# Optimization experiments

Measured on AMD Instinct MI355X. Metric: run time of the kernel, lower is better.

The kernel has to match this reference:

```python
import jax, jax.numpy as jnp
import numpy as np

BLANK = 1
NEG = -1e30


def ctc_loss_mean(logprobs, targets, input_lengths, target_lengths):
    """CTC loss, log-space forward DP, matching torch.nn.CTCLoss(blank=1, reduction='mean').
    logprobs: [B,T,V] log-softmaxed; targets: [B,L] int; lengths: [B] int."""
    B, T, V = logprobs.shape
    L = targets.shape[1]
    S = 2 * L + 1  # extended label seq: blank interleaved
    ext = jnp.full((B, S), BLANK, dtype=targets.dtype)
    ext = ext.at[:, 1::2].set(targets)
    # lp_ext[b,t,s] = logprobs[b,t,ext[b,s]]
    lp_ext = jnp.take_along_axis(logprobs, jnp.broadcast_to(ext[:, None, :], (B, T, S)), axis=2)
    ext_m2 = jnp.pad(ext, ((0, 0), (2, 0)), constant_values=BLANK)[:, :S]
    skip_ok = (ext != BLANK) & (ext != ext_m2)  # [B,S] allow s-2 transition

    alpha = jnp.full((B, S), NEG, dtype=logprobs.dtype)
    alpha = alpha.at[:, 0].set(lp_ext[:, 0, 0])
    alpha = alpha.at[:, 1].set(jnp.where(target_lengths > 0, lp_ext[:, 0, 1], NEG))

    def step(alpha, inp):
        lp_t, t = inp  # lp_t: [B,S]
        a1 = jnp.pad(alpha, ((0, 0), (1, 0)), constant_values=NEG)[:, :S]
        a2 = jnp.pad(alpha, ((0, 0), (2, 0)), constant_values=NEG)[:, :S]
        a2 = jnp.where(skip_ok, a2, NEG)
        new = jnp.logaddexp(jnp.logaddexp(alpha, a1), a2) + lp_t
        alpha = jnp.where((t < input_lengths)[:, None], new, alpha)
        return alpha, None

    lp_tbs = jnp.transpose(lp_ext, (1, 0, 2))  # [T,B,S]
    alpha, _ = jax.lax.scan(step, alpha, (lp_tbs[1:], jnp.arange(1, T)))

    idx_last = 2 * target_lengths  # final blank position
    idx_prev = jnp.maximum(idx_last - 1, 0)
    a_last = jnp.take_along_axis(alpha, idx_last[:, None], axis=1)[:, 0]
    a_prev = jnp.where(target_lengths > 0,
                       jnp.take_along_axis(alpha, idx_prev[:, None], axis=1)[:, 0], NEG)
    per_sample = -jnp.logaddexp(a_last, a_prev)
    tl = jnp.maximum(target_lengths, 1).astype(logprobs.dtype)
    return jnp.mean(per_sample / tl)  # torch 'mean': divide by target_len, then batch mean


def setup_inputs() -> dict:
    key = jax.random.key(0)
    ks = jax.random.split(key, 8)
    B, Ssrc, D, STRIDE, V, L = 32, 512, 512, 4, 512, 256
    representation = jax.random.normal(ks[0], (B, Ssrc, D), dtype=jnp.float32)
    encoder_mask = jnp.ones((B, Ssrc), dtype=bool)
    targets = jax.random.randint(ks[1], (B, L), 2, V)  # avoid blank=1 and 0
    target_mask = jnp.ones((B, L), dtype=bool)
    def lin(k, fin, fout):
        return jax.random.normal(k, (fin, fout), dtype=jnp.float32) / np.sqrt(fin)
    return {
        "representation": representation,
        "encoder_mask": encoder_mask,
        "targets": targets,
        "target_mask": target_mask,
        "W_exp": lin(ks[2], D, STRIDE * D),
        "b_exp": jnp.zeros((STRIDE * D,), jnp.float32),
        "W1": lin(ks[3], D, 2 * D),
        "b1": jnp.zeros((2 * D,), jnp.float32),
        "W2": lin(ks[4], 2 * D, V),
        "b2": jnp.zeros((V,), jnp.float32),
    }


def reference(representation, encoder_mask, targets, target_mask,
              W_exp, b_exp, W1, b1, W2, b2):
    B = representation.shape[0]
    dim = W_exp.shape[0]
    seq_lengths = encoder_mask.astype(jnp.int32).sum(1)
    stride = W_exp.shape[1] // dim
    # expand: Linear(dim, stride*dim) then fold stride into time axis
    states = (jnp.einsum("bsd,de->bse", representation, W_exp) + b_exp).reshape(B, -1, dim)
    h = jax.nn.relu(jnp.einsum("btd,dh->bth", states, W1) + b1)
    logits = jnp.einsum("bth,hv->btv", h, W2) + b2  # dropout: eval-mode identity
    logprobs = jax.nn.log_softmax(logits, axis=-1)
    target_lengths = target_mask.astype(jnp.int32).sum(1)
    out_lengths = stride * seq_lengths
    loss = ctc_loss_mean(logprobs, targets, out_lengths, target_lengths)
    loss = jnp.where(jnp.isnan(loss) | jnp.isinf(loss), jnp.zeros_like(loss), loss)
    return logprobs, out_lengths, loss
```

## Files before the change

### kernel.cpp

```cpp
#include <hip/hip_runtime.h>
#include <math.h>

#define B_ 32
#define SSRC 512
#define D_ 512
#define STRIDE_ 4
#define V_ 512
#define L_ 256
#define T_ (SSRC * STRIDE_)
#define S_ (2 * L_ + 1)
#define BLANKI 1
#define PSTRIDE 264
#define BOOST 4096.0f
#define BOOST_BITS 12

typedef __attribute__((ext_vector_type(8))) short bf16x8;
typedef __attribute__((ext_vector_type(4))) float f32x4;

__device__ __forceinline__ unsigned short bf16r(float x) {
    unsigned u = __float_as_uint(x);
    return (unsigned short)((u + 0x7fffu + ((u >> 16) & 1u)) >> 16);
}
__device__ __forceinline__ float bf2f(unsigned short u) {
    return __uint_as_float((unsigned)u << 16);
}
__device__ __forceinline__ void gl_lds16(const unsigned short* g, unsigned short* l) {
    __builtin_amdgcn_global_load_lds(
        (const __attribute__((address_space(1))) unsigned int*)g,
        (__attribute__((address_space(3))) unsigned int*)l, 16, 0, 0);
}

__global__ __launch_bounds__(256) void combine_bias(
    const float* __restrict__ b_exp, const float* __restrict__ W1,
    const float* __restrict__ b1, float* __restrict__ bc)
{
    int j = blockIdx.x * 256 + threadIdx.x;
    int k = j >> 10, h = j & 1023;
    float s = b1[h];
    const float* be = b_exp + k * 512;
    for (int d = 0; d < 512; ++d)
        s = fmaf(be[d], W1[d * 1024 + h], s);
    bc[j] = s;
}

__global__ __launch_bounds__(256) void transpose_cvt(
    const float* __restrict__ in, unsigned short* __restrict__ out, int R, int C)
{
    __shared__ float tile[32][33];
    int bx = blockIdx.x * 32, by = blockIdx.y * 32;
    int tx = threadIdx.x, ty = threadIdx.y;
#pragma unroll
    for (int i = 0; i < 32; i += 8)
        tile[ty + i][tx] = in[(size_t)(by + ty + i) * C + bx + tx];
    __syncthreads();
#pragma unroll
    for (int i = 0; i < 32; i += 8)
        out[(size_t)(bx + ty + i) * R + by + tx] = bf16r(tile[tx][ty + i]);
}

__global__ __launch_bounds__(256) void cvt_f32_bf16(
    const float* __restrict__ in, unsigned short* __restrict__ out, int n4)
{
    int i = blockIdx.x * 256 + threadIdx.x;
    if (i >= n4) return;
    float4 v = ((const float4*)in)[i];
    ushort4 o;
    o.x = bf16r(v.x); o.y = bf16r(v.y); o.z = bf16r(v.z); o.w = bf16r(v.w);
    ((ushort4*)out)[i] = o;
}

template <bool RELU, bool OUTBF16, bool BIAS>
__global__ __launch_bounds__(256) void gemm_mfma(
    const unsigned short* __restrict__ A, int lda, long zA,
    const unsigned short* __restrict__ BT, int ldb, long zBT,
    void* __restrict__ Cvoid, int ldc, long zC,
    const float* __restrict__ bias, int K)
{
    __shared__ unsigned short As[2][128][32];
    __shared__ unsigned short Bs[2][128][32];
    const int tid = threadIdx.x;
    const int wid = tid >> 6, lane = tid & 63;

    A  += (size_t)blockIdx.z * zA;
    BT += (size_t)blockIdx.z * zBT;
    unsigned short* Cb = OUTBF16 ? ((unsigned short*)Cvoid + (size_t)blockIdx.z * zC) : nullptr;
    float*          Cf = OUTBF16 ? nullptr : ((float*)Cvoid + (size_t)blockIdx.z * zC);

    const int gx = gridDim.x;
    int wg = blockIdx.y * gx + blockIdx.x;
    const int q = (gx * gridDim.y) >> 3;
    wg = (wg & 7) * q + (wg >> 3);
    const int bm = (wg / gx) * 128, bn = (wg % gx) * 128;

    const int wm = (wid >> 1) * 64, wn = (wid & 1) * 64;

    f32x4 acc[4][4] = {};
    const int r_in = lane >> 2;
    const int cch = (lane & 3) * 8;
    const int rbase = wid * 32;

    auto stage = [&](int buf, int k0) {
#pragma unroll
        for (int i = 0; i < 2; ++i) {
            int rloc = rbase + i * 16;
            gl_lds16(A  + (size_t)(bm + rloc + r_in) * lda + k0 + cch, &As[buf][rloc][0]);
            gl_lds16(BT + (size_t)(bn + rloc + r_in) * ldb + k0 + cch, &Bs[buf][rloc][0]);
        }
    };

    const int nt = K / 32;
    stage(0, 0);
    for (int t = 0; t < nt; ++t) {
        int cur = t & 1;
        __syncthreads();
        if (t + 1 < nt) stage(cur ^ 1, (t + 1) * 32);
        bf16x8 af[4], bfr[4];
#pragma unroll
        for (int mi = 0; mi < 4; ++mi)
            af[mi] = *(const bf16x8*)&As[cur][wm + mi * 16 + (lane & 15)][(lane >> 4) * 8];
#pragma unroll
        for (int ni = 0; ni < 4; ++ni)
            bfr[ni] = *(const bf16x8*)&Bs[cur][wn + ni * 16 + (lane & 15)][(lane >> 4) * 8];
#pragma unroll
        for (int mi = 0; mi < 4; ++mi)
#pragma unroll
            for (int ni = 0; ni < 4; ++ni)
                acc[mi][ni] = __builtin_amdgcn_mfma_f32_16x16x32_bf16(
                    af[mi], bfr[ni], acc[mi][ni], 0, 0, 0);
    }

#pragma unroll
    for (int ni = 0; ni < 4; ++ni) {
        int gcol = bn + wn + ni * 16 + (lane & 15);
        float bv = BIAS ? bias[gcol] : 0.f;
#pragma unroll
        for (int mi = 0; mi < 4; ++mi) {
#pragma unroll
            for (int q2 = 0; q2 < 4; ++q2) {
                int grow = bm + wm + mi * 16 + ((lane >> 4) << 2) + q2;
                float x = acc[mi][ni][q2] + bv;
                if (RELU) x = fmaxf(x, 0.f);
                if (OUTBF16)
                    Cb[(size_t)grow * ldc + gcol] = bf16r(x);
                else
                    Cf[(size_t)grow * ldc + gcol] = x;
            }
        }
    }
}

__global__ __launch_bounds__(512) void gemm2_lsm(
    const unsigned short* __restrict__ H,
    const unsigned short* __restrict__ W2T,
    const float* __restrict__ b2,
    float* __restrict__ lp)
{
    __shared__ __align__(16) char SMEM[81920];
    unsigned short* As = (unsigned short*)SMEM;
    unsigned short* Bs = (unsigned short*)(SMEM + 16384);
    float* redm = (float*)SMEM;
    float* reds = (float*)(SMEM + 2048);

    const int tid = threadIdx.x;
    const int wid = tid >> 6, lane = tid & 63;
    const int wr = wid >> 2, wc = wid & 3;
    const int r0 = blockIdx.x * 128;

    auto stage = [&](int buf, int k0) {
#pragma unroll
        for (int ii = 0; ii < 5; ++ii) {
            int issue = wid * 5 + ii;
            if (issue < 8) {
                int rr = issue * 16;
                gl_lds16(H + (size_t)(r0 + rr + (lane >> 2)) * 1024 + k0 + (lane & 3) * 8,
                         &As[buf * 4096 + rr * 32]);
            } else {
                int rr = (issue - 8) * 16;
                gl_lds16(W2T + (size_t)(rr + (lane >> 2)) * 1024 + k0 + (lane & 3) * 8,
                         &Bs[buf * 16384 + rr * 32]);
            }
        }
    };

    f32x4 acc[4][8] = {};
    stage(0, 0);
    for (int t = 0; t < 32; ++t) {
        const int cur = t & 1;
        __syncthreads();
        if (t + 1 < 32) stage(cur ^ 1, (t + 1) * 32);
        bf16x8 af[4], bfr[8];
#pragma unroll
        for (int mi = 0; mi < 4; ++mi)
            af[mi] = *(const bf16x8*)&As[cur * 4096 +
                        (wr * 64 + mi * 16 + (lane & 15)) * 32 + (lane >> 4) * 8];
#pragma unroll
        for (int ni = 0; ni < 8; ++ni)
            bfr[ni] = *(const bf16x8*)&Bs[cur * 16384 +
                        (wc * 128 + ni * 16 + (lane & 15)) * 32 + (lane >> 4) * 8];
#pragma unroll
        for (int mi = 0; mi < 4; ++mi)
#pragma unroll
            for (int ni = 0; ni < 8; ++ni)
                acc[mi][ni] = __builtin_amdgcn_mfma_f32_16x16x32_bf16(
                    af[mi], bfr[ni], acc[mi][ni], 0, 0, 0);
    }

    float bcol[8];
#pragma unroll
    for (int ni = 0; ni < 8; ++ni) bcol[ni] = b2[wc * 128 + ni * 16 + (lane & 15)];
#pragma unroll
    for (int mi = 0; mi < 4; ++mi)
#pragma unroll
        for (int ni = 0; ni < 8; ++ni)
#pragma unroll
            for (int q = 0; q < 4; ++q) acc[mi][ni][q] += bcol[ni];

    __syncthreads();

    float rm[4][4];
#pragma unroll
    for (int mi = 0; mi < 4; ++mi)
#pragma unroll
        for (int q = 0; q < 4; ++q) {
            float m = acc[mi][0][q];
#pragma unroll
            for (int ni = 1; ni < 8; ++ni) m = fmaxf(m, acc[mi][ni][q]);
#pragma unroll
            for (int off = 1; off < 16; off <<= 1) m = fmaxf(m, __shfl_xor(m, off));
            rm[mi][q] = m;
        }
    if ((lane & 15) == 0) {
#pragma unroll
        for (int mi = 0; mi < 4; ++mi)
#pragma unroll
            for (int q = 0; q < 4; ++q)
                redm[wc * 128 + wr * 64 + mi * 16 + ((lane >> 4) << 2) + q] = rm[mi][q];
    }
    __syncthreads();
#pragma unroll
    for (int mi = 0; mi < 4; ++mi)
#pragma unroll
        for (int q = 0; q < 4; ++q) {
            int row = wr * 64 + mi * 16 + ((lane >> 4) << 2) + q;
            rm[mi][q] = fmaxf(fmaxf(redm[0 * 128 + row], redm[1 * 128 + row]),
                              fmaxf(redm[2 * 128 + row], redm[3 * 128 + row]));
        }
    float rs[4][4];
#pragma unroll
    for (int mi = 0; mi < 4; ++mi)
#pragma unroll
        for (int q = 0; q < 4; ++q) {
            float s = 0.f;
#pragma unroll
            for (int ni = 0; ni < 8; ++ni) s += expf(acc[mi][ni][q] - rm[mi][q]);
#pragma unroll
            for (int off = 1; off < 16; off <<= 1) s += __shfl_xor(s, off);
            rs[mi][q] = s;
        }
    if ((lane & 15) == 0) {
#pragma unroll
        for (int mi = 0; mi < 4; ++mi)
#pragma unroll
            for (int q = 0; q < 4; ++q)
                reds[wc * 128 + wr * 64 + mi * 16 + ((lane >> 4) << 2) + q] = rs[mi][q];
    }
    __syncthreads();
#pragma unroll
    for (int mi = 0; mi < 4; ++mi)
#pragma unroll
        for (int q = 0; q < 4; ++q) {
            int row = wr * 64 + mi * 16 + ((lane >> 4) << 2) + q;
            float st = (reds[0 * 128 + row] + reds[1 * 128 + row]) +
                       (reds[2 * 128 + row] + reds[3 * 128 + row]);
            float lse = rm[mi][q] + logf(st);
#pragma unroll
            for (int ni = 0; ni < 8; ++ni) {
                int col = wc * 128 + ni * 16 + (lane & 15);
                lp[(size_t)(r0 + row) * 512 + col] = acc[mi][ni][q] - lse;
            }
        }
}

__global__ __launch_bounds__(256) void gather_p(
    const float* __restrict__ lp, const int* __restrict__ targets,
    unsigned short* __restrict__ P)
{
    const int w = (blockIdx.x << 2) + (threadIdx.x >> 6);
    const int l = threadIdx.x & 63;
    const int wl = threadIdx.x >> 6;
    const int b = w >> 11;

    __shared__ unsigned short pr[4][512];
    const float* row = lp + (size_t)w * 512;
    float4 v0 = ((const float4*)row)[l];
    float4 v1 = ((const float4*)row)[64 + l];
    pr[wl][l * 4 + 0] = bf16r(expf(v0.x) * BOOST);
    pr[wl][l * 4 + 1] = bf16r(expf(v0.y) * BOOST);
    pr[wl][l * 4 + 2] = bf16r(expf(v0.z) * BOOST);
    pr[wl][l * 4 + 3] = bf16r(expf(v0.w) * BOOST);
    pr[wl][256 + l * 4 + 0] = bf16r(expf(v1.x) * BOOST);
    pr[wl][256 + l * 4 + 1] = bf16r(expf(v1.y) * BOOST);
    pr[wl][256 + l * 4 + 2] = bf16r(expf(v1.z) * BOOST);
    pr[wl][256 + l * 4 + 3] = bf16r(expf(v1.w) * BOOST);
    __syncthreads();

    int4 tg = ((const int4*)(targets + (size_t)b * L_))[l];
    ushort4 o;
    o.x = pr[wl][tg.x]; o.y = pr[wl][tg.y]; o.z = pr[wl][tg.z]; o.w = pr[wl][tg.w];
    *(ushort4*)&P[(size_t)w * PSTRIDE + l * 4] = o;
    if (l == 0) P[(size_t)w * PSTRIDE + 256] = pr[wl][BLANKI];
}

struct Pr5 { float pb, p1, p3, p5, p7; };

__device__ __forceinline__ Pr5 ldrowf(const unsigned short* rp, int l)
{
    ushort4 q = *(const ushort4*)(rp + 4 * l);
    Pr5 r;
    r.pb = bf2f(rp[256]);
    r.p1 = bf2f(q.x); r.p3 = bf2f(q.y); r.p5 = bf2f(q.z); r.p7 = bf2f(q.w);
    return r;
}

#define REP16(OP) OP(0) OP(1) OP(2) OP(3) OP(4) OP(5) OP(6) OP(7) \
                  OP(8) OP(9) OP(10) OP(11) OP(12) OP(13) OP(14) OP(15)

__global__ __launch_bounds__(64) void ctc_fwd_bwd(
    const unsigned short* __restrict__ P,
    const int* __restrict__ enc_mask, const int* __restrict__ targets,
    const int* __restrict__ tgt_mask,
    float* __restrict__ out_len_f,
    double* __restrict__ AV, double* __restrict__ BV,
    int* __restrict__ EF, int* __restrict__ EB,
    int* __restrict__ ILv, int* __restrict__ tl_out)
{
    const int b = blockIdx.x & 31;
    const bool isf = blockIdx.x < 32;
    const int l = threadIdx.x;

    int se = 0, st = 0;
    {
        const int* em = enc_mask + (size_t)b * SSRC;
#pragma unroll
        for (int i = 0; i < 8; ++i) se += (em[i * 64 + l] != 0) ? 1 : 0;
        const int* tm = tgt_mask + (size_t)b * L_;
#pragma unroll
        for (int i = 0; i < 4; ++i) st += (tm[i * 64 + l] != 0) ? 1 : 0;
#pragma unroll
        for (int off = 32; off; off >>= 1) {
            se += __shfl_xor(se, off);
            st += __shfl_xor(st, off);
        }
    }
    const int tl = st;
    const int IL = STRIDE_ * se;
    const int h = (IL > 0) ? ((IL - 1) >> 1) : 0;

    const int4 tg = ((const int4*)(targets + (size_t)b * L_))[l];
    int prevw = __shfl_up(tg.w, 1);
    if (l == 0) prevw = BLANKI;
    const bool k1 = (tg.x != BLANKI) && (tg.x != prevw);
    const bool k3 = (tg.y != BLANKI) && (tg.y != tg.x);
    const bool k5 = (tg.z != BLANKI) && (tg.z != tg.y);
    const bool k7 = (tg.w != BLANKI) && (tg.w != tg.z);

    const unsigned short* Pb = P + (size_t)b * T_ * PSTRIDE;

    double a0 = 0, a1 = 0, a2 = 0, a3 = 0, a4 = 0, a5 = 0, a6 = 0, a7 = 0, a8 = 0;
    int Ei = 0;

    auto rescale9 = [&]() {
        double m = fmax(fmax(fmax(a0, a1), fmax(a2, a3)),
                        fmax(fmax(a4, a5), fmax(fmax(a6, a7), a8)));
        int e = (int)((__double_as_longlong(m) >> 52) & 0x7ff);
#pragma unroll
        for (int off = 1; off < 64; off <<= 1) {
            int o = __shfl_xor(e, off);
            e = o > e ? o : e;
        }
        int sh = 1023 - e;
        double sc = __longlong_as_double(((long long)(sh + 1023)) << 52);
        Ei += e - 1023;
        a0 *= sc; a1 *= sc; a2 *= sc; a3 *= sc; a4 *= sc;
        a5 *= sc; a6 *= sc; a7 *= sc; a8 *= sc;
    };

    if (isf) {
        if (l == 0) {
            a0 = (double)bf2f(Pb[256]);
            if (tl > 0) a1 = (double)bf2f(Pb[0]);
        }
        auto fstep = [&](const Pr5& r) {
            double pb = (double)r.pb, p1 = (double)r.p1, p3 = (double)r.p3;
            double p5 = (double)r.p5, p7 = (double)r.p7;
            double u1 = __shfl_up(a7, 1);
            if (l == 0) u1 = 0.0;
            double n0 = (a0 + u1) * pb;
            double n1 = (a0 + a1 + (k1 ? u1 : 0.0)) * p1;
            double n2 = (a1 + a2) * pb;
            double n3 = (a2 + a3 + (k3 ? a1 : 0.0)) * p3;
            double n4 = (a3 + a4) * pb;
            double n5 = (a4 + a5 + (k5 ? a3 : 0.0)) * p5;
            double n6 = (a5 + a6) * pb;
            double n7 = (a6 + a7 + (k7 ? a5 : 0.0)) * p7;
            double n8 = (l == 63) ? (a7 + a8) * pb : 0.0;
            a0 = n0; a1 = n1; a2 = n2; a3 = n3; a4 = n4;
            a5 = n5; a6 = n6; a7 = n7; a8 = n8;
        };
        const int nst = h;
        if (nst > 0) {
            Pr5 q0, q1, q2, q3, q4, q5, q6, q7, q8, q9, q10, q11, q12, q13, q14, q15;
#define LDI(i) { int ti = 1 + i; if (ti > nst) ti = nst; \
                 q##i = ldrowf(Pb + (size_t)ti * PSTRIDE, l); }
            REP16(LDI)
#undef LDI
            int t = 1;
            while (t + 15 <= nst) {
#define STP(i) { fstep(q##i); int ti = t + 16 + i; if (ti > nst) ti = nst; \
                 q##i = ldrowf(Pb + (size_t)ti * PSTRIDE, l); }
                REP16(STP)
#undef STP
                rescale9();
                t += 16;
            }
            int rem = nst - t + 1;
#define TLS(i) if (i < rem) fstep(q##i);
            REP16(TLS)
#undef TLS
        }
        rescale9();
        double* av = AV + b * 520;
        av[l * 8 + 0] = a0; av[l * 8 + 1] = a1; av[l * 8 + 2] = a2; av[l * 8 + 3] = a3;
        av[l * 8 + 4] = a4; av[l * 8 + 5] = a5; av[l * 8 + 6] = a6; av[l * 8 + 7] = a7;
        if (l == 63) av[512] = a8;
        if (l == 0) {
            EF[b] = Ei; ILv[b] = IL; tl_out[b] = tl;
            out_len_f[b] = (float)IL;
        }
    } else {
        {
            int s0 = l * 8;
            int e0 = 2 * tl, e1 = 2 * tl - 1;
            a0 = (s0 + 0 == e0 || (tl > 0 && s0 + 0 == e1)) ? 1.0 : 0.0;
            a1 = (s0 + 1 == e0 || (tl > 0 && s0 + 1 == e1)) ? 1.0 : 0.0;
            a2 = (s0 + 2 == e0 || (tl > 0 && s0 + 2 == e1)) ? 1.0 : 0.0;
            a3 = (s0 + 3 == e0 || (tl > 0 && s0 + 3 == e1)) ? 1.0 : 0.0;
            a4 = (s0 + 4 == e0 || (tl > 0 && s0 + 4 == e1)) ? 1.0 : 0.0;
            a5 = (s0 + 5 == e0 || (tl > 0 && s0 + 5 == e1)) ? 1.0 : 0.0;
            a6 = (s0 + 6 == e0 || (tl > 0 && s0 + 6 == e1)) ? 1.0 : 0.0;
            a7 = (s0 + 7 == e0 || (tl > 0 && s0 + 7 == e1)) ? 1.0 : 0.0;
            if (l == 63) a8 = (512 == e0) ? 1.0 : 0.0;
        }
        float knff = __shfl_down(k1 ? 1.f : 0.f, 1);
        if (l == 63) knff = 0.f;
        const double knf = (double)knff;
        auto bstep = [&](const Pr5& r) {
            double pb = (double)r.pb, p1 = (double)r.p1, p3 = (double)r.p3;
            double p5 = (double)r.p5, p7 = (double)r.p7;
            double g0 = a0 * pb, g1 = a1 * p1, g2 = a2 * pb, g3 = a3 * p3;
            double g4 = a4 * pb, g5 = a5 * p5, g6 = a6 * pb, g7 = a7 * p7;
            double g8 = (l == 63) ? a8 * pb : 0.0;
            double d1 = __shfl_down(g0, 1);
            double d2 = __shfl_down(g1, 1);
            if (l == 63) { d1 = g8; d2 = 0.0; }
            double m0 = g0 + g1;
            double m1 = g1 + g2 + (k3 ? g3 : 0.0);
            double m2 = g2 + g3;
            double m3 = g3 + g4 + (k5 ? g5 : 0.0);
            double m4 = g4 + g5;
            double m5 = g5 + g6 + (k7 ? g7 : 0.0);
            double m6 = g6 + g7;
            double m7 = g7 + d1 + knf * d2;
            double m8 = (l == 63) ? g8 : 0.0;
            a0 = m0; a1 = m1; a2 = m2; a3 = m3; a4 = m4;
            a5 = m5; a6 = m6; a7 = m7; a8 = m8;
        };
        const int nbs = IL - 1 - h;
        if (nbs > 0) {
            const int rmin = h + 1;
            Pr5 q0, q1, q2, q3, q4, q5, q6, q7, q8, q9, q10, q11, q12, q13, q14, q15;
#define LDB(i) { int ri = IL - 1 - i; if (ri < rmin) ri = rmin; \
                 q##i = ldrowf(Pb + (size_t)ri * PSTRIDE, l); }
            REP16(LDB)
#undef LDB
            int j = 0;
            while (j + 16 <= nbs) {
#define STB(i) { bstep(q##i); int ri = IL - 1 - (j + 16 + i); if (ri < rmin) ri = rmin; \
                 q##i = ldrowf(Pb + (size_t)ri * PSTRIDE, l); }
                REP16(STB)
#undef STB
                rescale9();
                j += 16;
            }
            int rem = nbs - j;
#define TLB(i) if (i < rem) bstep(q##i);
            REP16(TLB)
#undef TLB
        }
        rescale9();
        double* bv = BV + b * 520;
        bv[l * 8 + 0] = a0; bv[l * 8 + 1] = a1; bv[l * 8 + 2] = a2; bv[l * 8 + 3] = a3;
        bv[l * 8 + 4] = a4; bv[l * 8 + 5] = a5; bv[l * 8 + 6] = a6; bv[l * 8 + 7] = a7;
        if (l == 63) bv[512] = a8;
        if (l == 0) EB[b] = Ei;
    }
}

__global__ __launch_bounds__(64) void ctc_combine(
    const double* __restrict__ AV, const double* __restrict__ BV,
    const int* __restrict__ EF, const int* __restrict__ EB,
    const int* __restrict__ ILv, float* __restrict__ per_sample)
{
    const int b = blockIdx.x, l = threadIdx.x;
    const double* av = AV + b * 520;
    const double* bv = BV + b * 520;
    double s = 0.0;
#pragma unroll
    for (int i = 0; i < 8; ++i)
        s += av[l * 8 + i] * bv[l * 8 + i];
    if (l == 63) s += av[512] * bv[512];
#pragma unroll
    for (int off = 1; off < 64; off <<= 1) s += __shfl_xor(s, off);
    if (l == 0) {
        double lg = log(s) +
            (double)(EF[b] + EB[b] - BOOST_BITS * ILv[b]) * 0.6931471805599453;
        per_sample[b] = -(float)lg;
    }
}

__global__ __launch_bounds__(64) void ctc_loss_final(
    const float* __restrict__ per_sample, const int* __restrict__ tl,
    float* __restrict__ out_loss)
{
    int tid = threadIdx.x;
    float v = 0.f;
    if (tid < B_) {
        int t = tl[tid] < 1 ? 1 : tl[tid];
        v = per_sample[tid] / (float)t;
    }
#pragma unroll
    for (int off = 32; off; off >>= 1) v += __shfl_down(v, off);
    if (tid == 0) {
        float loss = v / (float)B_;
        if (isnan(loss) || isinf(loss)) loss = 0.f;
        *out_loss = loss;
    }
}

extern "C" void kernel_launch(void* const* d_in, const int* in_sizes, int n_in,
                              void* d_out, int out_size, void* d_ws, size_t ws_size,
                              hipStream_t stream)
{
    (void)in_sizes; (void)n_in; (void)out_size; (void)ws_size;

    const float* rep      = (const float*)d_in[0];
    const int*   enc_mask = (const int*)d_in[1];
    const int*   targets  = (const int*)d_in[2];
    const int*   tgt_mask = (const int*)d_in[3];
    const float* W_exp    = (const float*)d_in[4];
    const float* b_exp    = (const float*)d_in[5];
    const float* W1       = (const float*)d_in[6];
    const float* b1       = (const float*)d_in[7];
    const float* W2       = (const float*)d_in[8];
    const float* b2       = (const float*)d_in[9];

    float* out       = (float*)d_out;
    float* logprobs  = out;
    float* out_len_f = out + (size_t)B_ * T_ * V_;
    float* out_loss  = out_len_f + B_;
    unsigned short* Hd = (unsigned short*)d_out;

    unsigned short* WcT = (unsigned short*)d_ws;
    float* bc           = (float*)(WcT + (size_t)4096 * 512);
    float* per_sample   = bc + 4096;
    int*   tl_out       = (int*)(per_sample + 64);
    unsigned short* P   = (unsigned short*)(tl_out + 64);
    double* AV          = (double*)(P + (size_t)65536 * PSTRIDE);
    double* BV          = AV + 32 * 520;
    int*   EF           = (int*)(BV + 32 * 520);
    int*   EB           = EF + 32;
    int*   ILv          = EB + 32;
    unsigned short* repb   = P;
    unsigned short* W_expb = P + (size_t)16384 * 512;
    unsigned short* W1T    = W_expb + (size_t)512 * 2048;
    unsigned short* W2T    = WcT;

    cvt_f32_bf16<<<8192, 256, 0, stream>>>(rep, repb, (16384 * 512) / 4);
    cvt_f32_bf16<<<1024, 256, 0, stream>>>(W_exp, W_expb, (512 * 2048) / 4);
    transpose_cvt<<<dim3(32, 16), dim3(32, 8), 0, stream>>>(W1, W1T, 512, 1024);

    gemm_mfma<false, true, false><<<dim3(4, 8, 4), 256, 0, stream>>>(
        W1T, 512, 0, W_expb, 2048, 512, WcT, 512, (long)1024 * 512, nullptr, 512);
    combine_bias<<<16, 256, 0, stream>>>(b_exp, W1, b1, bc);

    gemm_mfma<true, true, true><<<dim3(32, 128), 256, 0, stream>>>(
        repb, 512, 0, WcT, 512, 0, Hd, 4096, 0, bc, 512);

    transpose_cvt<<<dim3(16, 32), dim3(32, 8), 0, stream>>>(W2, W2T, 1024, 512);

    gemm2_lsm<<<512, 512, 0, stream>>>(Hd, W2T, b2, logprobs);
    gather_p<<<(B_ * T_) / 4, 256, 0, stream>>>(logprobs, targets, P);

    ctc_fwd_bwd<<<64, 64, 0, stream>>>(P, enc_mask, targets, tgt_mask,
                                       out_len_f, AV, BV, EF, EB, ILv, tl_out);
    ctc_combine<<<32, 64, 0, stream>>>(AV, BV, EF, EB, ILv, per_sample);
    ctc_loss_final<<<1, 64, 0, stream>>>(per_sample, tl_out, out_loss);
}
```

Measured before the change: 421.2 us.

## Fuse CTC probability gather into GEMM2 log-softmax epilogue, widen to 16 waves

```diff
diff --git a/kernel.cpp b/kernel.cpp
--- a/kernel.cpp
+++ b/kernel.cpp
@@ -149,32 +149,37 @@
     }
 }
 
-__global__ __launch_bounds__(512) void gemm2_lsm(
+__global__ __launch_bounds__(1024) void gemm2_lsm(
     const unsigned short* __restrict__ H,
     const unsigned short* __restrict__ W2T,
     const float* __restrict__ b2,
-    float* __restrict__ lp)
+    const int* __restrict__ targets,
+    float* __restrict__ lp,
+    unsigned short* __restrict__ P)
 {
     __shared__ __align__(16) char SMEM[81920];
     unsigned short* As = (unsigned short*)SMEM;
     unsigned short* Bs = (unsigned short*)(SMEM + 16384);
     float* redm = (float*)SMEM;
-    float* reds = (float*)(SMEM + 2048);
+    float* reds = (float*)(SMEM + 4096);
+    unsigned short* prt = (unsigned short*)(SMEM + 8192);
+    int* s_tg = (int*)(SMEM + 8192 + 65536);
 
     const int tid = threadIdx.x;
     const int wid = tid >> 6, lane = tid & 63;
-    const int wr = wid >> 2, wc = wid & 3;
+    const int wr = wid >> 3, wc = wid & 7;
     const int r0 = blockIdx.x * 128;
+    const int b = r0 >> 11;
 
     auto stage = [&](int buf, int k0) {
 #pragma unroll
-        for (int ii = 0; ii < 5; ++ii) {
-            int issue = wid * 5 + ii;
+        for (int ii = 0; ii < 3; ++ii) {
+            int issue = wid + 16 * ii;
             if (issue < 8) {
                 int rr = issue * 16;
                 gl_lds16(H + (size_t)(r0 + rr + (lane >> 2)) * 1024 + k0 + (lane & 3) * 8,
                          &As[buf * 4096 + rr * 32]);
-            } else {
+            } else if (issue < 40) {
                 int rr = (issue - 8) * 16;
                 gl_lds16(W2T + (size_t)(rr + (lane >> 2)) * 1024 + k0 + (lane & 3) * 8,
                          &Bs[buf * 16384 + rr * 32]);
@@ -182,39 +187,40 @@
         }
     };
 
-    f32x4 acc[4][8] = {};
+    f32x4 acc[4][4] = {};
     stage(0, 0);
     for (int t = 0; t < 32; ++t) {
         const int cur = t & 1;
         __syncthreads();
         if (t + 1 < 32) stage(cur ^ 1, (t + 1) * 32);
-        bf16x8 af[4], bfr[8];
+        bf16x8 af[4], bfr[4];
 #pragma unroll
         for (int mi = 0; mi < 4; ++mi)
             af[mi] = *(const bf16x8*)&As[cur * 4096 +
                         (wr * 64 + mi * 16 + (lane & 15)) * 32 + (lane >> 4) * 8];
 #pragma unroll
-        for (int ni = 0; ni < 8; ++ni)
+        for (int ni = 0; ni < 4; ++ni)
             bfr[ni] = *(const bf16x8*)&Bs[cur * 16384 +
-                        (wc * 128 + ni * 16 + (lane & 15)) * 32 + (lane >> 4) * 8];
+                        (wc * 64 + ni * 16 + (lane & 15)) * 32 + (lane >> 4) * 8];
 #pragma unroll
         for (int mi = 0; mi < 4; ++mi)
 #pragma unroll
-            for (int ni = 0; ni < 8; ++ni)
+            for (int ni = 0; ni < 4; ++ni)
                 acc[mi][ni] = __builtin_amdgcn_mfma_f32_16x16x32_bf16(
                     af[mi], bfr[ni], acc[mi][ni], 0, 0, 0);
     }
 
-    float bcol[8];
-#pragma unroll
-    for (int ni = 0; ni < 8; ++ni) bcol[ni] = b2[wc * 128 + ni * 16 + (lane & 15)];
+    float bcol[4];
+#pragma unroll
+    for (int ni = 0; ni < 4; ++ni) bcol[ni] = b2[wc * 64 + ni * 16 + (lane & 15)];
 #pragma unroll
     for (int mi = 0; mi < 4; ++mi)
 #pragma unroll
-        for (int ni = 0; ni < 8; ++ni)
+        for (int ni = 0; ni < 4; ++ni)
 #pragma unroll
             for (int q = 0; q < 4; ++q) acc[mi][ni][q] += bcol[ni];
 
+    if (tid < 256) s_tg[tid] = targets[b * L_ + tid];
     __syncthreads();
 
     float rm[4][4];
@@ -224,7 +230,7 @@
         for (int q = 0; q < 4; ++q) {
             float m = acc[mi][0][q];
 #pragma unroll
-            for (int ni = 1; ni < 8; ++ni) m = fmaxf(m, acc[mi][ni][q]);
+            for (int ni = 1; ni < 4; ++ni) m = fmaxf(m, acc[mi][ni][q]);
 #pragma unroll
             for (int off = 1; off < 16; off <<= 1) m = fmaxf(m, __shfl_xor(m, off));
             rm[mi][q] = m;
@@ -242,8 +248,10 @@
 #pragma unroll
         for (int q = 0; q < 4; ++q) {
             int row = wr * 64 + mi * 16 + ((lane >> 4) << 2) + q;
-            rm[mi][q] = fmaxf(fmaxf(redm[0 * 128 + row], redm[1 * 128 + row]),
-                              fmaxf(redm[2 * 128 + row], redm[3 * 128 + row]));
+            float m = redm[row];
+#pragma unroll
+            for (int g = 1; g < 8; ++g) m = fmaxf(m, redm[g * 128 + row]);
+            rm[mi][q] = m;
         }
     float rs[4][4];
 #pragma unroll
@@ -252,7 +260,7 @@
         for (int q = 0; q < 4; ++q) {
             float s = 0.f;
 #pragma unroll
-            for (int ni = 0; ni < 8; ++ni) s += expf(acc[mi][ni][q] - rm[mi][q]);
+            for (int ni = 0; ni < 4; ++ni) s += expf(acc[mi][ni][q] - rm[mi][q]);
 #pragma unroll
             for (int off = 1; off < 16; off <<= 1) s += __shfl_xor(s, off);
             rs[mi][q] = s;
@@ -270,45 +278,41 @@
 #pragma unroll
         for (int q = 0; q < 4; ++q) {
             int row = wr * 64 + mi * 16 + ((lane >> 4) << 2) + q;
-            float st = (reds[0 * 128 + row] + reds[1 * 128 + row]) +
-                       (reds[2 * 128 + row] + reds[3 * 128 + row]);
-            float lse = rm[mi][q] + logf(st);
-#pragma unroll
-            for (int ni = 0; ni < 8; ++ni) {
-                int col = wc * 128 + ni * 16 + (lane & 15);
-                lp[(size_t)(r0 + row) * 512 + col] = acc[mi][ni][q] - lse;
-            }
-        }
-}
-
-__global__ __launch_bounds__(256) void gather_p(
-    const float* __restrict__ lp, const int* __restrict__ targets,
-    unsigned short* __restrict__ P)
-{
-    const int w = (blockIdx.x << 2) + (threadIdx.x >> 6);
-    const int l = threadIdx.x & 63;
-    const int wl = threadIdx.x >> 6;
-    const int b = w >> 11;
-
-    __shared__ unsigned short pr[4][512];
-    const float* row = lp + (size_t)w * 512;
-    float4 v0 = ((const float4*)row)[l];
-    float4 v1 = ((const float4*)row)[64 + l];
-    pr[wl][l * 4 + 0] = bf16r(expf(v0.x) * BOOST);
-    pr[wl][l * 4 + 1] = bf16r(expf(v0.y) * BOOST);
-    pr[wl][l * 4 + 2] = bf16r(expf(v0.z) * BOOST);
-    pr[wl][l * 4 + 3] = bf16r(expf(v0.w) * BOOST);
-    pr[wl][256 + l * 4 + 0] = bf16r(expf(v1.x) * BOOST);
-    pr[wl][256 + l * 4 + 1] = bf16r(expf(v1.y) * BOOST);
-    pr[wl][256 + l * 4 + 2] = bf16r(expf(v1.z) * BOOST);
-    pr[wl][256 + l * 4 + 3] = bf16r(expf(v1.w) * BOOST);
-    __syncthreads();
-
-    int4 tg = ((const int4*)(targets + (size_t)b * L_))[l];
-    ushort4 o;
-    o.x = pr[wl][tg.x]; o.y = pr[wl][tg.y]; o.z = pr[wl][tg.z]; o.w = pr[wl][tg.w];
-    *(ushort4*)&P[(size_t)w * PSTRIDE + l * 4] = o;
-    if (l == 0) P[(size_t)w * PSTRIDE + 256] = pr[wl][BLANKI];
+            float st = reds[row];
+#pragma unroll
+            for (int g = 1; g < 8; ++g) st += reds[g * 128 + row];
+            rm[mi][q] = rm[mi][q] + logf(st);
+        }
+
+#pragma unroll
+    for (int p = 0; p < 2; ++p) {
+        if (wr == p) {
+#pragma unroll
+            for (int mi = 0; mi < 4; ++mi)
+#pragma unroll
+                for (int q = 0; q < 4; ++q) {
+                    int rloc = mi * 16 + ((lane >> 4) << 2) + q;
+                    int row = wr * 64 + rloc;
+#pragma unroll
+                    for (int ni = 0; ni < 4; ++ni) {
+                        int col = wc * 64 + ni * 16 + (lane & 15);
+                        float lpv = acc[mi][ni][q] - rm[mi][q];
+                        lp[(size_t)(r0 + row) * 512 + col] = lpv;
+                        prt[rloc * 512 + col] = bf16r(expf(lpv) * BOOST);
+                    }
+                }
+        }
+        __syncthreads();
+        if (tid < 514) {
+            int j = tid % 257;
+            int rh = tid / 257;
+            int col = (j < 256) ? s_tg[j] : BLANKI;
+#pragma unroll 4
+            for (int r = rh * 32; r < rh * 32 + 32; ++r)
+                P[(size_t)(r0 + p * 64 + r) * PSTRIDE + j] = prt[r * 512 + col];
+        }
+        __syncthreads();
+    }
 }
 
 struct Pr5 { float pb, p1, p3, p5, p7; };
@@ -325,7 +329,7 @@
 #define REP16(OP) OP(0) OP(1) OP(2) OP(3) OP(4) OP(5) OP(6) OP(7) \
                   OP(8) OP(9) OP(10) OP(11) OP(12) OP(13) OP(14) OP(15)
 
-__global__ __launch_bounds__(64) void ctc_fwd_bwd(
+__global__ __launch_bounds__(512) void ctc_fwd_bwd(
     const unsigned short* __restrict__ P,
     const int* __restrict__ enc_mask, const int* __restrict__ targets,
     const int* __restrict__ tgt_mask,
@@ -334,9 +338,11 @@
     int* __restrict__ EF, int* __restrict__ EB,
     int* __restrict__ ILv, int* __restrict__ tl_out)
 {
-    const int b = blockIdx.x & 31;
-    const bool isf = blockIdx.x < 32;
-    const int l = threadIdx.x;
+    const int wid = threadIdx.x >> 6;
+    const int l = threadIdx.x & 63;
+    const int task = blockIdx.x * 8 + wid;
+    const int b = task & 31;
+    const bool isf = task < 32;
 
     int se = 0, st = 0;
     {
@@ -598,10 +604,9 @@
 
     transpose_cvt<<<dim3(16, 32), dim3(32, 8), 0, stream>>>(W2, W2T, 1024, 512);
 
-    gemm2_lsm<<<512, 512, 0, stream>>>(Hd, W2T, b2, logprobs);
-    gather_p<<<(B_ * T_) / 4, 256, 0, stream>>>(logprobs, targets, P);
-
-    ctc_fwd_bwd<<<64, 64, 0, stream>>>(P, enc_mask, targets, tgt_mask,
+    gemm2_lsm<<<512, 1024, 0, stream>>>(Hd, W2T, b2, targets, logprobs, P);
+
+    ctc_fwd_bwd<<<8, 512, 0, stream>>>(P, enc_mask, targets, tgt_mask,
                                        out_len_f, AV, BV, EF, EB, ILv, tl_out);
     ctc_combine<<<32, 64, 0, stream>>>(AV, BV, EF, EB, ILv, per_sample);
     ctc_loss_final<<<1, 64, 0, stream>>>(per_sample, tl_out, out_loss);
```

Result: slower. 488.1 us (+15.9%).
